# Optimization experiments

Measured on AMD Instinct MI355X. Metric: run time of the kernel, lower is better.

The kernel has to match this reference:

```python
import jax, jax.numpy as jnp
import numpy as np

D_MODEL = 1024
NUM_HEADS = 16
HEAD_DIM = D_MODEL // NUM_HEADS
B, T = 2, 2048


def setup_inputs() -> dict:
    key = jax.random.key(0)
    k1, k2, k3, k4, k5 = jax.random.split(key, 5)
    s = 1.0 / np.sqrt(D_MODEL)
    x = jax.random.normal(k1, (B, T, D_MODEL), dtype=jnp.float32)
    mask = jnp.ones((B, T), dtype=jnp.int32)
    W_qkv = jax.random.uniform(k2, (D_MODEL, 3 * D_MODEL), jnp.float32, -s, s)
    b_qkv = jax.random.uniform(k3, (3 * D_MODEL,), jnp.float32, -s, s)
    W_out = jax.random.uniform(k4, (D_MODEL, D_MODEL), jnp.float32, -s, s)
    b_out = jax.random.uniform(k5, (D_MODEL,), jnp.float32, -s, s)
    return {"x": x, "mask": mask, "W_qkv": W_qkv, "b_qkv": b_qkv,
            "W_out": W_out, "b_out": b_out}


def reference(x, mask, W_qkv, b_qkv, W_out, b_out):
    Bv, Tv, Dv = x.shape
    scale = HEAD_DIM ** -0.5
    qkv = x @ W_qkv + b_qkv                       # [B,T,3D]
    qkv = qkv.reshape(Bv, Tv, 3, NUM_HEADS, HEAD_DIM)
    qkv = jnp.transpose(qkv, (2, 0, 3, 1, 4))     # [3,B,H,T,hd]
    q, k, v = qkv[0], qkv[1], qkv[2]
    scores = jnp.einsum('bhqd,bhkd->bhqk', q, k) * scale  # [B,H,T,T]
    m = mask[:, None, None, :]                    # [B,1,1,T]
    scores = jnp.where(m == 0, -jnp.inf, scores)
    attn = jax.nn.softmax(scores, axis=-1)
    out = jnp.einsum('bhqk,bhkd->bhqd', attn, v)  # [B,H,T,hd]
    out = jnp.transpose(out, (0, 2, 1, 3)).reshape(Bv, Tv, Dv)
    return out @ W_out + b_out
```

## Files before the change

kernel.cpp:

```cpp
#include <hip/hip_runtime.h>

typedef __bf16 bf16;
typedef __bf16 bf16x8 __attribute__((ext_vector_type(8)));
typedef __bf16 bf16x4 __attribute__((ext_vector_type(4)));
typedef float  f32x4  __attribute__((ext_vector_type(4)));
typedef float  f32x16 __attribute__((ext_vector_type(16)));
typedef unsigned int u32x4 __attribute__((ext_vector_type(4)));

#define MFMA16(a, b, c) __builtin_amdgcn_mfma_f32_16x16x32_bf16((a), (b), (c), 0, 0, 0)
#define MFMA32(a, b, c) __builtin_amdgcn_mfma_f32_32x32x16_bf16((a), (b), (c), 0, 0, 0)

__device__ __forceinline__ float fexp2(float x) {
  return __builtin_amdgcn_exp2f(x);
}

__device__ __forceinline__ unsigned cvt_pk_bf16(float lo, float hi) {
  unsigned r;
  asm("v_cvt_pk_bf16_f32 %0, %1, %2" : "=v"(r) : "v"(lo), "v"(hi));
  return r;
}

__device__ __forceinline__ void gload_lds16(const bf16* g, bf16* l) {
  __builtin_amdgcn_global_load_lds(
      (const __attribute__((address_space(1))) void*)g,
      (__attribute__((address_space(3))) void*)l, 16, 0, 0);
}


__global__ __launch_bounds__(256) void cast_bf16_kernel(
    const float* __restrict__ in, bf16* __restrict__ out, int n4) {
  int i = blockIdx.x * 256 + threadIdx.x;
  if (i < n4) {
    float4 v = reinterpret_cast<const float4*>(in)[i];
    bf16x4 o;
    o[0] = (bf16)v.x; o[1] = (bf16)v.y; o[2] = (bf16)v.z; o[3] = (bf16)v.w;
    reinterpret_cast<bf16x4*>(out)[i] = o;
  }
}

__global__ __launch_bounds__(256) void transpose_cast_kernel(
    const float* __restrict__ W, bf16* __restrict__ Wt, int K, int N) {
  __shared__ bf16 tile[64 * 66];
  const int k0 = blockIdx.y * 64, n0 = blockIdx.x * 64;
  const int c = threadIdx.x & 63, rb = threadIdx.x >> 6;
#pragma unroll
  for (int p = 0; p < 16; ++p) {
    int r = p * 4 + rb;
    tile[c * 66 + r] = (bf16)W[(long)(k0 + r) * N + n0 + c];
  }
  __syncthreads();
#pragma unroll
  for (int p = 0; p < 16; ++p) {
    int r = p * 4 + rb;
    Wt[(long)(n0 + r) * K + k0 + c] = tile[r * 66 + c];
  }
}

template <int EPI>
__global__ __launch_bounds__(256, 2) void gemm_bt(
    const bf16* __restrict__ A, const bf16* __restrict__ Bt,
    const float* __restrict__ bias, bf16* __restrict__ oQ,
    bf16* __restrict__ oK, bf16* __restrict__ oVT, float* __restrict__ oC,
    int K) {
  __shared__ bf16 As[128 * 64];
  __shared__ bf16 Bs[128 * 64];
  const int tid = threadIdx.x, lane = tid & 63, wid = tid >> 6;
  const int wr = wid >> 1, wc = wid & 1;
  const int brow = blockIdx.x * 128, bcol = blockIdx.y * 128;
  const int srow = lane >> 3, scol8 = (lane & 7) * 8;
  const int c15 = lane & 15, g = lane >> 4;

  f32x4 acc[4][4];
#pragma unroll
  for (int m = 0; m < 4; ++m)
#pragma unroll
    for (int n = 0; n < 4; ++n) acc[m][n] = f32x4{0.f, 0.f, 0.f, 0.f};

  const bf16* Ab = A + (long)brow * K + scol8;
  const bf16* Bb = Bt + (long)bcol * K + scol8;

  for (int k0 = 0; k0 < K; k0 += 64) {
#pragma unroll
    for (int i = 0; i < 4; ++i) {
      int c = wid * 4 + i;
      int row = c * 8 + srow;
      gload_lds16(Ab + (long)row * K + k0, &As[c * 512]);
    }
#pragma unroll
    for (int i = 0; i < 4; ++i) {
      int c = wid * 4 + i;
      int row = c * 8 + srow;
      gload_lds16(Bb + (long)row * K + k0, &Bs[c * 512]);
    }
    __syncthreads();
#pragma unroll
    for (int kk = 0; kk < 64; kk += 32) {
      bf16x8 a[4], b[4];
#pragma unroll
      for (int m = 0; m < 4; ++m)
        a[m] = *(const bf16x8*)&As[(wr * 64 + m * 16 + c15) * 64 + kk + g * 8];
#pragma unroll
      for (int n = 0; n < 4; ++n)
        b[n] = *(const bf16x8*)&Bs[(wc * 64 + n * 16 + c15) * 64 + kk + g * 8];
#pragma unroll
      for (int m = 0; m < 4; ++m)
#pragma unroll
        for (int n = 0; n < 4; ++n)
          acc[m][n] = MFMA16(a[m], b[n], acc[m][n]);
    }
    __syncthreads();
  }

#pragma unroll
  for (int n = 0; n < 4; ++n) {
    const int col = bcol + wc * 64 + n * 16 + c15;
    const float bv = bias[col];
    if (EPI == 0) {
      const int which = col >> 10, wi = col & 1023, h = wi >> 6, d = wi & 63;
      const float sc = (which == 0) ? 0.18033688011112042f : 1.0f;
#pragma unroll
      for (int m = 0; m < 4; ++m) {
        const int row0 = brow + wr * 64 + m * 16 + g * 4;
        const int bb = row0 >> 11, t0 = row0 & 2047;
        const long hb = bb * 16 + h;
        if (which == 2) {
          bf16x4 pv;
#pragma unroll
          for (int r = 0; r < 4; ++r) pv[r] = (bf16)(acc[m][n][r] + bv);
          *(bf16x4*)&oVT[(hb * 64 + d) * 2048 + t0] = pv;
        } else {
          bf16* dst = ((which == 0) ? oQ : oK) + (hb * 2048 + t0) * 64 + d;
#pragma unroll
          for (int r = 0; r < 4; ++r)
            dst[(long)r * 64] = (bf16)((acc[m][n][r] + bv) * sc);
        }
      }
    } else {
#pragma unroll
      for (int m = 0; m < 4; ++m) {
        const long row = brow + wr * 64 + m * 16 + g * 4;
#pragma unroll
        for (int r = 0; r < 4; ++r) oC[(row + r) * 1024 + col] = acc[m][n][r] + bv;
      }
    }
  }
}

__global__ __launch_bounds__(512, 4) void attn_kernel(
    const bf16* __restrict__ Q, const bf16* __restrict__ K,
    const bf16* __restrict__ VT, const int* __restrict__ mask,
    bf16* __restrict__ Aout) {
  __shared__ bf16 Kl[2][2][4096];
  __shared__ bf16 Vl[2][2][4096];
  __shared__ float sws[8][32];
  __shared__ float mlL[2][4][2][32];
  const int tid = threadIdx.x, lane = tid & 63, w = tid >> 6;
  const int wq = w & 3, s = w >> 2;
  const int col = lane & 31, hi = lane >> 5, c7 = col & 7;
  const int bid = blockIdx.x;
  const int swz = (bid & 7) * 64 + (bid >> 3);
  const int bh = swz >> 4, qb = swz & 15;
  const int b = bh >> 4, h = bh & 15;
  const int q0 = qb * 128 + wq * 32;
  const int koff0 = s * 1024;

  const bf16* Kbase = K + (long)bh * 2048 * 64;
  const bf16* Vbase = VT + (long)bh * 64 * 2048;
  const int* mb = mask + b * 2048;

  const int srow = lane >> 3;
  const int xoff = ((lane & 7) ^ srow) << 3;

  auto stage = [&](int buf, int t) {
    const int koff = koff0 + t * 64;
#pragma unroll
    for (int i = 0; i < 2; ++i) {
      const int c = wq * 2 + i;
      gload_lds16(Kbase + (long)(koff + c * 8 + srow) * 64 + xoff,
                  &Kl[s][buf][c * 512]);
      gload_lds16(Vbase + (long)(c * 8 + srow) * 2048 + koff + xoff,
                  &Vl[s][buf][c * 512]);
    }
  };

  const bf16* Qp = Q + ((long)bh * 2048 + q0 + col) * 64 + hi * 8;
  bf16x8 bq[4];
#pragma unroll
  for (int dc = 0; dc < 4; ++dc) bq[dc] = *(const bf16x8*)(Qp + dc * 16);

  f32x16 o0, o1;
#pragma unroll
  for (int r = 0; r < 16; ++r) { o0[r] = 0.f; o1[r] = 0.f; }
  float mrun = -1e30f, lrun = 0.f;

  stage(0, 0);
  for (int t = 0; t < 16; ++t) {
    const int cur = t & 1;
    __builtin_amdgcn_s_barrier();
    const int mvA = mb[koff0 + t * 64 + col];
    const int mvB = mb[koff0 + t * 64 + 32 + col];
    if (t < 15) {
      stage(cur ^ 1, t + 1);
      asm volatile("s_waitcnt vmcnt(6)" ::: "memory");
    } else {
      asm volatile("s_waitcnt vmcnt(0)" ::: "memory");
    }
    __builtin_amdgcn_s_barrier();

#pragma unroll
    for (int sub = 0; sub < 2; ++sub) {
      const int mv = (sub == 0) ? mvA : mvB;
      const bf16* Krow = &Kl[s][cur][(sub * 32 + col) * 64];
      bf16x8 ak0 = *(const bf16x8*)(Krow + (((0 + hi) ^ c7) << 3));
      bf16x8 ak1 = *(const bf16x8*)(Krow + (((2 + hi) ^ c7) << 3));
      bf16x8 ak2 = *(const bf16x8*)(Krow + (((4 + hi) ^ c7) << 3));
      bf16x8 ak3 = *(const bf16x8*)(Krow + (((6 + hi) ^ c7) << 3));
      f32x16 st;
#pragma unroll
      for (int r = 0; r < 16; ++r) st[r] = 0.f;
      __builtin_amdgcn_s_setprio(1);
      st = MFMA32(ak0, bq[0], st);
      st = MFMA32(ak1, bq[1], st);
      st = MFMA32(ak2, bq[2], st);
      st = MFMA32(ak3, bq[3], st);
      __builtin_amdgcn_s_setprio(0);
      unsigned km32 = (unsigned)__ballot(mv != 0);
      if (km32 != 0xffffffffu) {
        unsigned km = km32 >> (hi * 4);
#pragma unroll
        for (int r = 0; r < 16; ++r)
          if (!((km >> ((r & 3) + 8 * (r >> 2))) & 1)) st[r] = -1e30f;
      }
      float m01 = fmaxf(st[0], st[1]), m23 = fmaxf(st[2], st[3]);
      float m45 = fmaxf(st[4], st[5]), m67 = fmaxf(st[6], st[7]);
      float m89 = fmaxf(st[8], st[9]), mab = fmaxf(st[10], st[11]);
      float mcd = fmaxf(st[12], st[13]), mef = fmaxf(st[14], st[15]);
      float m0 = fmaxf(fmaxf(fmaxf(m01, m23), fmaxf(m45, m67)),
                       fmaxf(fmaxf(m89, mab), fmaxf(mcd, mef)));
      if (__any(m0 > mrun + 8.0f)) {
        float pm = fmaxf(m0, __shfl_xor(m0, 32));
        float mnew = fmaxf(mrun, pm);
        float scale = fexp2(mrun - mnew);
        mrun = mnew;
        lrun *= scale;
        if (hi == 0) sws[w][col] = scale;
        asm volatile("s_waitcnt lgkmcnt(0)" ::: "memory");
#pragma unroll
        for (int r = 0; r < 16; ++r) {
          float sc = sws[w][(r & 3) + 8 * (r >> 2) + 4 * hi];
          o0[r] *= sc; o1[r] *= sc;
        }
      }
#pragma unroll
      for (int r = 0; r < 16; ++r) st[r] = fexp2(st[r] - mrun);
      float s01 = st[0] + st[1], s23 = st[2] + st[3], s45 = st[4] + st[5];
      float s67 = st[6] + st[7], s89 = st[8] + st[9], sab = st[10] + st[11];
      float scd = st[12] + st[13], sef = st[14] + st[15];
      lrun += ((s01 + s23) + (s45 + s67)) + ((s89 + sab) + (scd + sef));
      unsigned d0 = cvt_pk_bf16(st[0], st[1]);
      unsigned d1 = cvt_pk_bf16(st[2], st[3]);
      unsigned d2 = cvt_pk_bf16(st[4], st[5]);
      unsigned d3 = cvt_pk_bf16(st[6], st[7]);
      unsigned d4 = cvt_pk_bf16(st[8], st[9]);
      unsigned d5 = cvt_pk_bf16(st[10], st[11]);
      unsigned d6 = cvt_pk_bf16(st[12], st[13]);
      unsigned d7 = cvt_pk_bf16(st[14], st[15]);
      unsigned g02 = (unsigned)__shfl_xor((int)(hi ? d0 : d2), 32);
      unsigned g13 = (unsigned)__shfl_xor((int)(hi ? d1 : d3), 32);
      unsigned g46 = (unsigned)__shfl_xor((int)(hi ? d4 : d6), 32);
      unsigned g57 = (unsigned)__shfl_xor((int)(hi ? d5 : d7), 32);
      u32x4 w0 = {hi ? g02 : d0, hi ? g13 : d1, hi ? d2 : g02, hi ? d3 : g13};
      u32x4 w1 = {hi ? g46 : d4, hi ? g57 : d5, hi ? d6 : g46, hi ? d7 : g57};
      bf16x8 pa0 = __builtin_bit_cast(bf16x8, w0);
      bf16x8 pa1 = __builtin_bit_cast(bf16x8, w1);
      const bf16* Vrow0 = &Vl[s][cur][col * 64];
      const bf16* Vrow1 = &Vl[s][cur][(col + 32) * 64];
      const int g0 = ((sub * 4 + hi) ^ c7) << 3;
      const int g1 = ((sub * 4 + 2 + hi) ^ c7) << 3;
      bf16x8 bv00 = *(const bf16x8*)(Vrow0 + g0);
      bf16x8 bv10 = *(const bf16x8*)(Vrow0 + g1);
      bf16x8 bv01 = *(const bf16x8*)(Vrow1 + g0);
      bf16x8 bv11 = *(const bf16x8*)(Vrow1 + g1);
      __builtin_amdgcn_s_setprio(1);
      o0 = MFMA32(pa0, bv00, o0);
      o0 = MFMA32(pa1, bv10, o0);
      o1 = MFMA32(pa0, bv01, o1);
      o1 = MFMA32(pa1, bv11, o1);
      __builtin_amdgcn_s_setprio(0);
    }
  }

  lrun += __shfl_xor(lrun, 32);
  if (hi == 0) { mlL[s][wq][0][col] = mrun; mlL[s][wq][1][col] = lrun; }
  __syncthreads();

  float* Ol = (float*)Kl;
  if (s == 1) {
#pragma unroll
    for (int r = 0; r < 16; ++r) {
      Ol[(wq * 16 + r) * 128 + lane] = o0[r];
      Ol[(wq * 16 + r) * 128 + 64 + lane] = o1[r];
    }
  }
  __syncthreads();

  if (s == 0) {
#pragma unroll
    for (int r = 0; r < 16; ++r) {
      const int qr = (r & 3) + 8 * (r >> 2) + 4 * hi;
      float m0v = mlL[0][wq][0][qr], l0v = mlL[0][wq][1][qr];
      float m1v = mlL[1][wq][0][qr], l1v = mlL[1][wq][1][qr];
      float ms = fmaxf(m0v, m1v);
      float w0v = fexp2(m0v - ms), w1v = fexp2(m1v - ms);
      float inv = 1.0f / (w0v * l0v + w1v * l1v);
      float v0 = (w0v * o0[r] + w1v * Ol[(wq * 16 + r) * 128 + lane]) * inv;
      float v1 = (w0v * o1[r] + w1v * Ol[(wq * 16 + r) * 128 + 64 + lane]) * inv;
      long base = ((long)b * 2048 + q0 + qr) * 1024 + h * 64 + col;
      Aout[base] = (bf16)v0;
      Aout[base + 32] = (bf16)v1;
    }
  }
}

extern "C" void kernel_launch(void* const* d_in, const int* in_sizes, int n_in,
                              void* d_out, int out_size, void* d_ws,
                              size_t ws_size, hipStream_t stream) {
  const float* x    = (const float*)d_in[0];
  const int*   mask = (const int*)d_in[1];
  const float* Wqkv = (const float*)d_in[2];
  const float* bqkv = (const float*)d_in[3];
  const float* Wout = (const float*)d_in[4];
  const float* bout = (const float*)d_in[5];
  float* out = (float*)d_out;

  char* ws = (char*)d_ws;
  bf16* xb    = (bf16*)(ws);
  bf16* wqkvT = (bf16*)(ws + (8u << 20));
  bf16* woutT = (bf16*)(ws + (14u << 20));
  bf16* Qb    = (bf16*)(ws + (16u << 20));
  bf16* Kb    = (bf16*)(ws + (24u << 20));
  bf16* VTb   = (bf16*)(ws + (32u << 20));
  bf16* Aatt  = xb;

  cast_bf16_kernel<<<4096, 256, 0, stream>>>(x, xb, (4096 * 1024) / 4);
  transpose_cast_kernel<<<dim3(48, 16), 256, 0, stream>>>(Wqkv, wqkvT, 1024, 3072);
  transpose_cast_kernel<<<dim3(16, 16), 256, 0, stream>>>(Wout, woutT, 1024, 1024);
  gemm_bt<0><<<dim3(32, 24), 256, 0, stream>>>(xb, wqkvT, bqkv, Qb, Kb, VTb,
                                               nullptr, 1024);
  attn_kernel<<<512, 512, 0, stream>>>(Qb, Kb, VTb, mask, Aatt);
  gemm_bt<1><<<dim3(32, 8), 256, 0, stream>>>(Aatt, woutT, bout, nullptr,
                                              nullptr, nullptr, out, 1024);
}
```

Baseline: 133.1 us.

## Rewrite QKV projection GEMM as 256x256 double-buffered pipelined kernel

Replaces the templated 128x128 GEMM for the QKV projection with a dedicated 256x256-tile, 512-thread kernel. It double-buffers LDS with a swizzled layout, issues the next tile's direct-to-LDS loads in stages between MFMA phases, and raises wave priority around the MFMA bursts. Blocks are remapped for L2 locality. This aims to hide global load latency and raise data reuse per tile, at the cost of 128KB of LDS, more register pressure, and only 192 blocks, which may underfill the CUs. The output projection keeps the old kernel, now split out as its own function.

```diff
diff --git a/kernel.cpp b/kernel.cpp
--- a/kernel.cpp
+++ b/kernel.cpp
@@ -56,12 +56,118 @@
   }
 }
 
-template <int EPI>
-__global__ __launch_bounds__(256, 2) void gemm_bt(
+__global__ __launch_bounds__(512, 2) void gemm_qkv_256(
     const bf16* __restrict__ A, const bf16* __restrict__ Bt,
     const float* __restrict__ bias, bf16* __restrict__ oQ,
-    bf16* __restrict__ oK, bf16* __restrict__ oVT, float* __restrict__ oC,
-    int K) {
+    bf16* __restrict__ oK, bf16* __restrict__ oVT) {
+  __shared__ bf16 As[2][256 * 64];
+  __shared__ bf16 Bs[2][256 * 64];
+  const int tid = threadIdx.x, lane = tid & 63, w = tid >> 6;
+  const int wm = w >> 2, wn = w & 3;
+  const int bid = blockIdx.x;
+  const int swz = (bid & 7) * 24 + (bid >> 3);
+  const int brow = (swz & 15) * 256, bcol = (swz >> 4) * 256;
+  const int c15 = lane & 15, g = lane >> 4;
+  const int srow = lane >> 3;
+  const int xoff = ((lane & 7) ^ srow) << 3;
+
+  auto stage_half = [&](int buf, int t, int h, bool isB) {
+    const bf16* src = isB ? Bt : A;
+    const int rb = isB ? bcol : brow;
+    bf16* dst = isB ? &Bs[buf][0] : &As[buf][0];
+#pragma unroll
+    for (int i = 0; i < 2; ++i) {
+      const int c = w * 2 + i;
+      gload_lds16(src + (long)(rb + h * 128 + c * 8 + srow) * 1024 + t * 64 + xoff,
+                  dst + (h * 128 + c * 8) * 64);
+    }
+  };
+
+  f32x4 acc[8][4];
+#pragma unroll
+  for (int mi = 0; mi < 8; ++mi)
+#pragma unroll
+    for (int n = 0; n < 4; ++n) acc[mi][n] = f32x4{0.f, 0.f, 0.f, 0.f};
+
+  stage_half(0, 0, 0, false); stage_half(0, 0, 0, true);
+  stage_half(0, 0, 1, false); stage_half(0, 0, 1, true);
+
+  bf16x8 bfr[4];
+  for (int t = 0; t < 16; ++t) {
+    const int cur = t & 1;
+    __builtin_amdgcn_s_barrier();
+    if (t < 15) {
+      stage_half(cur ^ 1, t + 1, 0, false);
+      asm volatile("s_waitcnt vmcnt(2)" ::: "memory");
+    } else {
+      asm volatile("s_waitcnt vmcnt(0)" ::: "memory");
+    }
+    __builtin_amdgcn_s_barrier();
+
+#pragma unroll
+    for (int p = 0; p < 4; ++p) {
+      const int mh = p & 1, kh = p >> 1;
+      if (p == 0 || p == 2) {
+#pragma unroll
+        for (int n = 0; n < 4; ++n) {
+          const int rowB = wn * 64 + n * 16 + c15;
+          bfr[n] = *(const bf16x8*)&Bs[cur][rowB * 64 +
+                                            (((kh * 4 + g) ^ (rowB & 7)) << 3)];
+        }
+      }
+      bf16x8 afr[4];
+#pragma unroll
+      for (int m = 0; m < 4; ++m) {
+        const int rowA = wm * 128 + mh * 64 + m * 16 + c15;
+        afr[m] = *(const bf16x8*)&As[cur][rowA * 64 +
+                                          (((kh * 4 + g) ^ (rowA & 7)) << 3)];
+      }
+      if (t < 15) {
+        if (p == 1) stage_half(cur ^ 1, t + 1, 0, true);
+        else if (p == 2) stage_half(cur ^ 1, t + 1, 1, false);
+        else if (p == 3) stage_half(cur ^ 1, t + 1, 1, true);
+      }
+      __builtin_amdgcn_s_barrier();
+      __builtin_amdgcn_s_setprio(1);
+#pragma unroll
+      for (int m = 0; m < 4; ++m)
+#pragma unroll
+        for (int n = 0; n < 4; ++n)
+          acc[mh * 4 + m][n] = MFMA16(afr[m], bfr[n], acc[mh * 4 + m][n]);
+      __builtin_amdgcn_s_setprio(0);
+      if (p < 3) __builtin_amdgcn_s_barrier();
+    }
+  }
+
+#pragma unroll
+  for (int n = 0; n < 4; ++n) {
+    const int col = bcol + wn * 64 + n * 16 + c15;
+    const float bv = bias[col];
+    const int which = col >> 10, wi = col & 1023, h = wi >> 6, d = wi & 63;
+    const float sc = (which == 0) ? 0.18033688011112042f : 1.0f;
+#pragma unroll
+    for (int mi = 0; mi < 8; ++mi) {
+      const int row0 = brow + wm * 128 + mi * 16 + g * 4;
+      const int bb = row0 >> 11, t0 = row0 & 2047;
+      const long hb = bb * 16 + h;
+      if (which == 2) {
+        bf16x4 pv;
+#pragma unroll
+        for (int r = 0; r < 4; ++r) pv[r] = (bf16)(acc[mi][n][r] + bv);
+        *(bf16x4*)&oVT[(hb * 64 + d) * 2048 + t0] = pv;
+      } else {
+        bf16* dst = ((which == 0) ? oQ : oK) + (hb * 2048 + t0) * 64 + d;
+#pragma unroll
+        for (int r = 0; r < 4; ++r)
+          dst[(long)r * 64] = (bf16)((acc[mi][n][r] + bv) * sc);
+      }
+    }
+  }
+}
+
+__global__ __launch_bounds__(256, 2) void gemm_out(
+    const bf16* __restrict__ A, const bf16* __restrict__ Bt,
+    const float* __restrict__ bias, float* __restrict__ oC, int K) {
   __shared__ bf16 As[128 * 64];
   __shared__ bf16 Bs[128 * 64];
   const int tid = threadIdx.x, lane = tid & 63, wid = tid >> 6;
@@ -115,33 +221,11 @@
   for (int n = 0; n < 4; ++n) {
     const int col = bcol + wc * 64 + n * 16 + c15;
     const float bv = bias[col];
-    if (EPI == 0) {
-      const int which = col >> 10, wi = col & 1023, h = wi >> 6, d = wi & 63;
-      const float sc = (which == 0) ? 0.18033688011112042f : 1.0f;
-#pragma unroll
-      for (int m = 0; m < 4; ++m) {
-        const int row0 = brow + wr * 64 + m * 16 + g * 4;
-        const int bb = row0 >> 11, t0 = row0 & 2047;
-        const long hb = bb * 16 + h;
-        if (which == 2) {
-          bf16x4 pv;
-#pragma unroll
-          for (int r = 0; r < 4; ++r) pv[r] = (bf16)(acc[m][n][r] + bv);
-          *(bf16x4*)&oVT[(hb * 64 + d) * 2048 + t0] = pv;
-        } else {
-          bf16* dst = ((which == 0) ? oQ : oK) + (hb * 2048 + t0) * 64 + d;
-#pragma unroll
-          for (int r = 0; r < 4; ++r)
-            dst[(long)r * 64] = (bf16)((acc[m][n][r] + bv) * sc);
-        }
-      }
-    } else {
-#pragma unroll
-      for (int m = 0; m < 4; ++m) {
-        const long row = brow + wr * 64 + m * 16 + g * 4;
-#pragma unroll
-        for (int r = 0; r < 4; ++r) oC[(row + r) * 1024 + col] = acc[m][n][r] + bv;
-      }
+#pragma unroll
+    for (int m = 0; m < 4; ++m) {
+      const long row = brow + wr * 64 + m * 16 + g * 4;
+#pragma unroll
+      for (int r = 0; r < 4; ++r) oC[(row + r) * 1024 + col] = acc[m][n][r] + bv;
     }
   }
 }
@@ -345,9 +429,7 @@
   cast_bf16_kernel<<<4096, 256, 0, stream>>>(x, xb, (4096 * 1024) / 4);
   transpose_cast_kernel<<<dim3(48, 16), 256, 0, stream>>>(Wqkv, wqkvT, 1024, 3072);
   transpose_cast_kernel<<<dim3(16, 16), 256, 0, stream>>>(Wout, woutT, 1024, 1024);
-  gemm_bt<0><<<dim3(32, 24), 256, 0, stream>>>(xb, wqkvT, bqkv, Qb, Kb, VTb,
-                                               nullptr, 1024);
+  gemm_qkv_256<<<192, 512, 0, stream>>>(xb, wqkvT, bqkv, Qb, Kb, VTb);
   attn_kernel<<<512, 512, 0, stream>>>(Qb, Kb, VTb, mask, Aatt);
-  gemm_bt<1><<<dim3(32, 8), 256, 0, stream>>>(Aatt, woutT, bout, nullptr,
-                                              nullptr, nullptr, out, 1024);
-}
+  gemm_out<<<dim3(32, 8), 256, 0, stream>>>(Aatt, woutT, bout, out, 1024);
+}
```

Measured after the change: 143.1 us. 1.07x slower.
